# Optimization experiments

Hardware: AMD Instinct MI355X
Metric: run time of the kernel (lower is better)

Reference implementation:

```python
import jax, jax.numpy as jnp
import numpy as np

N_CODES = 8192
CODE_DIM = 256
COMMITMENT_COST = 0.25
DECAY = 0.99
EPS = 1e-05


def setup_inputs() -> dict:
    key = jax.random.key(0)
    k1, k2 = jax.random.split(key)
    z = jax.random.normal(k1, (8, 4096, CODE_DIM), dtype=jnp.float32)
    bound = 1.0 / N_CODES
    codebook_weight = jax.random.uniform(k2, (N_CODES, CODE_DIM), dtype=jnp.float32,
                                         minval=-bound, maxval=bound)
    ema_count = jnp.zeros((N_CODES,), dtype=jnp.float32)
    ema_weight = codebook_weight  # initialized as a clone of the codebook
    return {"z": z, "codebook_weight": codebook_weight,
            "ema_count": ema_count, "ema_weight": ema_weight}


def reference(z, codebook_weight, ema_count, ema_weight):
    B, L, D = z.shape
    flat_z = z.reshape(-1, D)                      # (N, D)
    # squared-distance matrix: ||z||^2 - 2 z.C^T + ||C||^2  -> (N, n_codes)
    dists = (jnp.sum(flat_z * flat_z, axis=1, keepdims=True)
             - 2.0 * flat_z @ codebook_weight.T
             + jnp.sum(codebook_weight * codebook_weight, axis=1)[None, :])
    indices = jnp.argmin(dists, axis=-1)           # (N,)
    z_q_flat = codebook_weight[indices]            # (N, D) gather

    # --- EMA codebook update (training-mode, no-grad branch) ---
    fz = jax.lax.stop_gradient(flat_z)
    count = jax.ops.segment_sum(jnp.ones_like(indices, dtype=jnp.float32),
                                indices, num_segments=N_CODES)          # one_hot.sum(0)
    new_ema_count = DECAY * ema_count + (1.0 - DECAY) * count
    weight_sum = jax.ops.segment_sum(fz, indices, num_segments=N_CODES)  # one_hot.T @ flat_z
    new_ema_weight = DECAY * ema_weight + (1.0 - DECAY) * weight_sum
    n = jnp.sum(new_ema_count)
    count_stable = (new_ema_count + EPS) / (n + N_CODES * EPS) * n
    new_codebook = new_ema_weight / count_stable[:, None]

    # --- losses + straight-through ---
    commitment_loss = jnp.mean((flat_z - jax.lax.stop_gradient(z_q_flat)) ** 2)
    vq_loss = COMMITMENT_COST * commitment_loss
    z_q_flat = flat_z + jax.lax.stop_gradient(z_q_flat - flat_z)
    z_q = z_q_flat.reshape(B, L, D)
    indices = indices.reshape(B, L)
    return (z_q, indices, vq_loss, new_codebook, new_ema_count, new_ema_weight)
```

## Files before the change

kernel.cpp:

```cpp
#include <hip/hip_runtime.h>
#include <stdint.h>

#define NROWS   32768
#define NCODES  8192
#define DIM     256
#define NSPLIT  8
#define CPS     1024
#define MAXFIX  24576
#define MAXPAIRS 262144
#define MAXRESC (MAXFIX * NSPLIT)

typedef __attribute__((ext_vector_type(8))) _Float16 f16x8;
typedef __attribute__((ext_vector_type(4))) float f32x4;

__device__ __forceinline__ f16x8 cvt8h(const float* __restrict__ p) {
    float4 a = *(const float4*)p;
    float4 b = *(const float4*)(p + 4);
    f16x8 H;
    H[0] = (_Float16)a.x; H[1] = (_Float16)a.y;
    H[2] = (_Float16)a.z; H[3] = (_Float16)a.w;
    H[4] = (_Float16)b.x; H[5] = (_Float16)b.y;
    H[6] = (_Float16)b.z; H[7] = (_Float16)b.w;
    return H;
}

__global__ __launch_bounds__(256) void k_prep(const float* __restrict__ cb,
                                              const float* __restrict__ z,
                                              unsigned short* __restrict__ bh,
                                              unsigned* __restrict__ cmax2,
                                              float* __restrict__ sum1) {
    __shared__ float zz[32 * 257];
    const int t = threadIdx.x;
    if (blockIdx.x < 1024) {
        int i = blockIdx.x * 256 + t;
        const float* p = cb + (size_t)i * 8;
        float4 a = *(const float4*)p;
        float4 b = *(const float4*)(p + 4);
        f16x8 H;
        H[0] = (_Float16)(a.x * 8192.0f); H[1] = (_Float16)(a.y * 8192.0f);
        H[2] = (_Float16)(a.z * 8192.0f); H[3] = (_Float16)(a.w * 8192.0f);
        H[4] = (_Float16)(b.x * 8192.0f); H[5] = (_Float16)(b.y * 8192.0f);
        H[6] = (_Float16)(b.z * 8192.0f); H[7] = (_Float16)(b.w * 8192.0f);
        int j = (i & ~31) | ((i & 31) ^ ((i >> 5) & 7));
        *(f16x8*)(bh + (size_t)j * 8) = H;
        float ss = a.x*a.x + a.y*a.y + a.z*a.z + a.w*a.w
                 + b.x*b.x + b.y*b.y + b.z*b.z + b.w*b.w;
        #pragma unroll
        for (int off = 1; off < 32; off <<= 1) ss += __shfl_xor(ss, off);
        if ((t & 31) == 0) atomicMax(cmax2, __float_as_uint(ss));
        return;
    }
    const int bid = blockIdx.x - 1024;
    const size_t base = (size_t)bid * 32 * 256;
    #pragma unroll
    for (int k = 0; k < 8; ++k) {
        int f4 = t + k * 256;
        float4 v = *(const float4*)(z + base + (size_t)f4 * 4);
        int row = f4 >> 6, col = (f4 & 63) * 4;
        float* d = &zz[row * 257 + col];
        d[0] = v.x * v.x; d[1] = v.y * v.y; d[2] = v.z * v.z; d[3] = v.w * v.w;
    }
    __syncthreads();
    if (t < 32) {
        const float* x = &zz[t * 257];
        float tot = 0.0f;
        #pragma unroll
        for (int h = 0; h < 2; ++h) {
            float r0 = x[0], r1 = x[1], r2 = x[2], r3 = x[3];
            float r4 = x[4], r5 = x[5], r6 = x[6], r7 = x[7];
            for (int i = 8; i < 128; i += 8) {
                r0 += x[i + 0]; r1 += x[i + 1]; r2 += x[i + 2]; r3 += x[i + 3];
                r4 += x[i + 4]; r5 += x[i + 5]; r6 += x[i + 6]; r7 += x[i + 7];
            }
            float bsum = ((r0 + r1) + (r2 + r3)) + ((r4 + r5) + (r6 + r7));
            tot = (h == 0) ? bsum : (tot + bsum);
            x += 128;
        }
        sum1[bid * 32 + t] = tot;
    }
}

__device__ __forceinline__ void stage_h(const unsigned short* __restrict__ gh,
                                        int cbase, int w, int lane,
                                        unsigned short* B) {
    const unsigned short* sh = gh + (size_t)cbase * 256;
    #pragma unroll
    for (int k = 0; k < 4; ++k) {
        const int ub = k * 256 + w * 64;
        __builtin_amdgcn_global_load_lds(
            (const __attribute__((address_space(1))) void*)(sh + (size_t)(ub + lane) * 8),
            (__attribute__((address_space(3))) void*)(B + (size_t)ub * 8), 16, 0, 0);
    }
}

__global__ __launch_bounds__(256, 2) void k_dist(
    const float* __restrict__ z,
    const unsigned short* __restrict__ bh,
    float* __restrict__ pm1, float* __restrict__ pm2, float* __restrict__ pm3)
{
    __shared__ __align__(16) unsigned short Bs[2][32][256];

    const int bid   = blockIdx.x;
    const int split = bid & (NSPLIT - 1);
    const int rt    = bid >> 3;
    const int rowbase = rt * 256;
    const int cbase0  = split * CPS;

    const int t    = threadIdx.x;
    const int w    = t >> 6;
    const int lane = t & 63;
    const int quad = lane >> 4;
    const int l15  = lane & 15;

    stage_h(bh, cbase0, w, lane, &Bs[0][0][0]);

    f16x8 Af[4][8];
    const int rbase = rowbase + w * 64;
    #pragma unroll
    for (int mt = 0; mt < 4; ++mt) {
        const float* zp = z + (size_t)(rbase + mt*16 + l15) * DIM + quad * 8;
        #pragma unroll
        for (int ks = 0; ks < 8; ++ks)
            Af[mt][ks] = cvt8h(zp + ks * 32);
    }

    int offB[2][8];
    #pragma unroll
    for (int nt = 0; nt < 2; ++nt) {
        const int cc = nt * 16 + l15;
        const int cx = cc & 7;
        #pragma unroll
        for (int ks = 0; ks < 8; ++ks)
            offB[nt][ks] = cc * 512 + (((quad + 4 * ks) ^ cx) * 16);
    }
    const unsigned idx0 = 8191u - (unsigned)(cbase0 + l15);

    float m1[16], m2[16], m3[16];
    #pragma unroll
    for (int s = 0; s < 16; ++s) { m1[s] = -3.4e38f; m2[s] = -3.4e38f; m3[s] = -3.4e38f; }

    __syncthreads();

#define KD_ROUND(RND, BCUR, BNXT)                                               \
    {                                                                           \
        if ((RND) + 1 < CPS / 32)                                               \
            stage_h(bh, cbase0 + ((RND) + 1) * 32, w, lane, (BNXT));            \
        const char* baseB = (const char*)(BCUR);                                \
        _Pragma("unroll")                                                       \
        for (int nt = 0; nt < 2; ++nt) {                                        \
            f32x4 a0 = {0,0,0,0}, a1 = {0,0,0,0}, a2 = {0,0,0,0}, a3 = {0,0,0,0};\
            _Pragma("unroll")                                                   \
            for (int ks = 0; ks < 8; ++ks) {                                    \
                f16x8 Bk = *(const f16x8*)(baseB + offB[nt][ks]);               \
                a0 = __builtin_amdgcn_mfma_f32_16x16x32_f16(Af[0][ks], Bk, a0, 0, 0, 0); \
                a1 = __builtin_amdgcn_mfma_f32_16x16x32_f16(Af[1][ks], Bk, a1, 0, 0, 0); \
                a2 = __builtin_amdgcn_mfma_f32_16x16x32_f16(Af[2][ks], Bk, a2, 0, 0, 0); \
                a3 = __builtin_amdgcn_mfma_f32_16x16x32_f16(Af[3][ks], Bk, a3, 0, 0, 0); \
            }                                                                   \
            const unsigned ibnt = idx0 - (unsigned)((RND) * 32 + nt * 16);      \
            _Pragma("unroll")                                                   \
            for (int mt = 0; mt < 4; ++mt) {                                    \
                _Pragma("unroll")                                               \
                for (int r = 0; r < 4; ++r) {                                   \
                    float dot = mt == 0 ? a0[r] : mt == 1 ? a1[r] : mt == 2 ? a2[r] : a3[r]; \
                    unsigned kb = (__float_as_uint(dot) & 0xFFFFE000u) | ibnt;  \
                    float kf = __uint_as_float(kb);                             \
                    int s = mt * 4 + r;                                         \
                    m3[s] = __builtin_amdgcn_fmed3f(m2[s], m3[s], kf);          \
                    m2[s] = __builtin_amdgcn_fmed3f(m1[s], m2[s], kf);          \
                    m1[s] = fmaxf(m1[s], kf);                                   \
                }                                                               \
            }                                                                   \
        }                                                                       \
        __syncthreads();                                                        \
    }

    for (int r2 = 0; r2 < CPS / 64; ++r2) {
        KD_ROUND(2 * r2,     &Bs[0][0][0], &Bs[1][0][0]);
        KD_ROUND(2 * r2 + 1, &Bs[1][0][0], &Bs[0][0][0]);
    }
#undef KD_ROUND

    #pragma unroll
    for (int off = 1; off < 16; off <<= 1) {
        #pragma unroll
        for (int s = 0; s < 16; ++s) {
            float o1 = __shfl_xor(m1[s], off);
            float o2 = __shfl_xor(m2[s], off);
            float o3 = __shfl_xor(m3[s], off);
            m3[s] = __builtin_amdgcn_fmed3f(m2[s], m3[s], o1);
            m2[s] = __builtin_amdgcn_fmed3f(m1[s], m2[s], o1);
            m1[s] = fmaxf(m1[s], o1);
            m3[s] = __builtin_amdgcn_fmed3f(m2[s], m3[s], o2);
            m2[s] = __builtin_amdgcn_fmed3f(m1[s], m2[s], o2);
            m1[s] = fmaxf(m1[s], o2);
            m3[s] = __builtin_amdgcn_fmed3f(m2[s], m3[s], o3);
            m2[s] = __builtin_amdgcn_fmed3f(m1[s], m2[s], o3);
            m1[s] = fmaxf(m1[s], o3);
        }
    }
    if (l15 == 0) {
        #pragma unroll
        for (int s = 0; s < 16; ++s) {
            int mt = s >> 2, r = s & 3;
            int row = rbase + mt * 16 + quad * 4 + r;
            pm1[row * NSPLIT + split] = m1[s];
            pm2[row * NSPLIT + split] = m2[s];
            pm3[row * NSPLIT + split] = m3[s];
        }
    }
}

__global__ void k_combine(const float* __restrict__ pm1, const float* __restrict__ pm2,
                          const float* __restrict__ pm3, const float* __restrict__ sum1,
                          const unsigned* __restrict__ cmax2,
                          int* __restrict__ idx_i, float* __restrict__ out_idx,
                          int* __restrict__ flagc, int* __restrict__ fixl,
                          float* __restrict__ fixthr, int* __restrict__ npairs,
                          int2* __restrict__ pairs, int* __restrict__ nresc,
                          int2* __restrict__ resc, int* __restrict__ count)
{
    int r = blockIdx.x * 256 + threadIdx.x;
    float a[8], b[8], c[8];
    #pragma unroll
    for (int s = 0; s < NSPLIT; ++s) {
        a[s] = pm1[r * NSPLIT + s];
        b[s] = pm2[r * NSPLIT + s];
        c[s] = pm3[r * NSPLIT + s];
    }
    float M1 = -3.4e38f, M2 = -3.4e38f;
    #pragma unroll
    for (int s = 0; s < NSPLIT; ++s) {
        M2 = fmaxf(fmaxf(M2, b[s]), fminf(M1, a[s]));
        M1 = fmaxf(M1, a[s]);
    }
    int I1 = (int)(8191u - (__float_as_uint(M1) & 8191u));
    idx_i[r] = I1;
    out_idx[r] = (float)I1;
    float cn = sqrtf(__uint_as_float(*cmax2)) * 8192.0f;
    float ds = 9.80e-4f * sqrtf(sum1[r]) * cn + 3e-3f;
    float t1 = sum1[r] - M1 * 0x1p-12f;
    unsigned eb = (__float_as_uint(t1 + 0.05f) >> 23) & 0xFFu;
    float q = __uint_as_float((eb - 23u) << 23);
    bool fixed = false;
    if (M1 - M2 <= (q + 2e-6f) * 8192.0f + 2.0f * ds + 0.0655f) {
        int p = atomicAdd(flagc, 1);
        if (p < MAXFIX) {
            fixed = true;
            fixl[p] = r;
            float thr = M1 - ((1.25f * q + 4e-6f) * 8192.0f + 2.2f * ds + 0.16f);
            fixthr[p] = thr;
            #pragma unroll
            for (int s = 0; s < NSPLIT; ++s) {
                if (a[s] >= thr) {
                    int pp = atomicAdd(npairs, 1);
                    if (pp < MAXPAIRS)
                        pairs[pp] = make_int2(p, (int)(8191u - (__float_as_uint(a[s]) & 8191u)));
                }
                if (b[s] >= thr) {
                    int pp = atomicAdd(npairs, 1);
                    if (pp < MAXPAIRS)
                        pairs[pp] = make_int2(p, (int)(8191u - (__float_as_uint(b[s]) & 8191u)));
                }
                if (c[s] >= thr) {
                    int pp = atomicAdd(npairs, 1);
                    if (pp < MAXPAIRS)
                        pairs[pp] = make_int2(p, (int)(8191u - (__float_as_uint(c[s]) & 8191u)));
                    int q2 = atomicAdd(nresc, 1);
                    if (q2 < MAXRESC) resc[q2] = make_int2(p, s);
                }
            }
        }
    }
    if (!fixed) atomicAdd(&count[I1], 1);
}

__global__ __launch_bounds__(256) void k_resc(
    const float* __restrict__ z, const float* __restrict__ cb,
    const int* __restrict__ nresc_p, const int2* __restrict__ resc,
    const int* __restrict__ fixl, const float* __restrict__ fixthr,
    int* __restrict__ npairs, int2* __restrict__ pairs)
{
    int nr = *nresc_p; if (nr > MAXRESC) nr = MAXRESC;
    const int w = threadIdx.x >> 6, lane = threadIdx.x & 63;
    for (int it = blockIdx.x; it < nr; it += gridDim.x) {
        const int slot = resc[it].x, split = resc[it].y;
        const int row = fixl[slot];
        const float thr = fixthr[slot];
        float4 zv = *(const float4*)(z + (size_t)row * DIM + lane * 4);
        const int cbase = split * CPS + w * 256;
        for (int cc = 0; cc < 256; cc += 4) {
            const float* cp = cb + (size_t)(cbase + cc) * DIM + lane * 4;
            float4 c0 = *(const float4*)(cp);
            float4 c1 = *(const float4*)(cp + DIM);
            float4 c2 = *(const float4*)(cp + 2 * DIM);
            float4 c3 = *(const float4*)(cp + 3 * DIM);
            float d0 = zv.x*c0.x + zv.y*c0.y + zv.z*c0.z + zv.w*c0.w;
            float d1 = zv.x*c1.x + zv.y*c1.y + zv.z*c1.z + zv.w*c1.w;
            float d2 = zv.x*c2.x + zv.y*c2.y + zv.z*c2.z + zv.w*c2.w;
            float d3 = zv.x*c3.x + zv.y*c3.y + zv.z*c3.z + zv.w*c3.w;
            #pragma unroll
            for (int off = 1; off < 64; off <<= 1) {
                d0 += __shfl_xor(d0, off);
                d1 += __shfl_xor(d1, off);
                d2 += __shfl_xor(d2, off);
                d3 += __shfl_xor(d3, off);
            }
            if (lane == 0) {
                if (d0 * 8192.0f >= thr) {
                    int pp = atomicAdd(npairs, 1);
                    if (pp < MAXPAIRS) pairs[pp] = make_int2(slot, cbase + cc);
                }
                if (d1 * 8192.0f >= thr) {
                    int pp = atomicAdd(npairs, 1);
                    if (pp < MAXPAIRS) pairs[pp] = make_int2(slot, cbase + cc + 1);
                }
                if (d2 * 8192.0f >= thr) {
                    int pp = atomicAdd(npairs, 1);
                    if (pp < MAXPAIRS) pairs[pp] = make_int2(slot, cbase + cc + 2);
                }
                if (d3 * 8192.0f >= thr) {
                    int pp = atomicAdd(npairs, 1);
                    if (pp < MAXPAIRS) pairs[pp] = make_int2(slot, cbase + cc + 3);
                }
            }
        }
    }
}

__global__ __launch_bounds__(256) void k_exact(
    const float* __restrict__ z, const float* __restrict__ cb,
    const float* __restrict__ sum1, const int* __restrict__ npairs_p,
    const int2* __restrict__ pairs, const int* __restrict__ fixl,
    unsigned long long* __restrict__ slotkey)
{
    int np = *npairs_p; if (np > MAXPAIRS) np = MAXPAIRS;
    const int lane = threadIdx.x & 63;
    const int wid = blockIdx.x * 4 + (threadIdx.x >> 6);
    for (int p = wid; p < np; p += gridDim.x * 4) {
        const int slot = pairs[p].x, code = pairs[p].y;
        const int row = fixl[slot];
        float4 a = *(const float4*)(z  + (size_t)row  * DIM + lane * 4);
        float4 c = *(const float4*)(cb + (size_t)code * DIM + lane * 4);
        double d = (double)a.x * (double)c.x + (double)a.y * (double)c.y
                 + (double)a.z * (double)c.z + (double)a.w * (double)c.w;
        #pragma unroll
        for (int off = 1; off < 64; off <<= 1) d += __shfl_xor(d, off);
        if (lane == 0) {
            float v = sum1[row] - 2.0f * (float)d;
            unsigned long long key =
                ((unsigned long long)__float_as_uint(v) << 32) | (unsigned)code;
            atomicMin(&slotkey[slot], key);
        }
    }
}

__global__ void k_fin(const int* __restrict__ flagc, const int* __restrict__ fixl,
                      const unsigned long long* __restrict__ slotkey,
                      int* __restrict__ idx_i, float* __restrict__ out_idx,
                      int* __restrict__ count)
{
    int nf = *flagc; if (nf > MAXFIX) nf = MAXFIX;
    int slot = blockIdx.x * 256 + threadIdx.x;
    if (slot >= nf) return;
    int r = fixl[slot];
    unsigned long long key = slotkey[slot];
    int idx;
    if (key != ~0ull) {
        idx = (int)(key & 0xFFFFFFFFull) & (NCODES - 1);
        idx_i[r] = idx;
        out_idx[r] = (float)idx;
    } else {
        idx = idx_i[r] & (NCODES - 1);
    }
    atomicAdd(&count[idx], 1);
}

__global__ __launch_bounds__(256) void k_prefix(const int* __restrict__ count,
                                                const float* __restrict__ in_ec,
                                                int* __restrict__ binstart,
                                                int* __restrict__ bincur,
                                                float* __restrict__ necs,
                                                float* __restrict__ out_nec,
                                                float* __restrict__ n_cell)
{
    __shared__ int ts[257];
    __shared__ float red[256];
    const int t = threadIdx.x;
    int local[32];
    int s = 0;
    float ecs = 0.0f;
    #pragma unroll
    for (int k = 0; k < 32; ++k) {
        int i = t * 32 + k;
        local[k] = count[i];
        s += local[k];
        float e = in_ec[i];
        ecs += e;
        float nec = fmaf(0.99f, e, 0.01f * (float)local[k]);
        necs[i] = nec;
        out_nec[i] = nec;
    }
    ts[t + 1] = s;
    if (t == 0) ts[0] = 0;
    red[t] = ecs;
    __syncthreads();
    for (int off = 1; off < 256; off <<= 1) {
        int v = (t >= off) ? ts[t + 1 - off] : 0;
        __syncthreads();
        ts[t + 1] += v;
        __syncthreads();
    }
    int base = ts[t];
    #pragma unroll
    for (int k = 0; k < 32; ++k) {
        int i = t * 32 + k;
        binstart[i] = base;
        bincur[i]   = base;
        base += local[k];
    }
    for (int off = 128; off > 0; off >>= 1) {
        __syncthreads();
        if (t < off) red[t] += red[t + off];
    }
    __syncthreads();
    if (t == 0) *n_cell = fmaf(0.99f, red[0], 0.01f * 32768.0f);
}

__global__ void k_place(const int* __restrict__ idx_i, int* __restrict__ bincur,
                        int* __restrict__ sorted)
{
    int row = blockIdx.x * 256 + threadIdx.x;
    int idx = idx_i[row] & (NCODES - 1);
    int pos = atomicAdd(&bincur[idx], 1);
    sorted[pos] = row;
}

__global__ __launch_bounds__(256) void k_wg(
    const float* __restrict__ z, const float* __restrict__ cb,
    const int* __restrict__ binstart, const int* __restrict__ count,
    const int* __restrict__ sorted, const float* __restrict__ in_ew,
    const float* __restrict__ necs, const float* __restrict__ n_cell,
    float* __restrict__ lossp, int* __restrict__ done,
    float* __restrict__ out_zq, float* __restrict__ out_ncb,
    float* __restrict__ out_new, float* __restrict__ out_loss)
{
    __shared__ int islast;
    __shared__ float lred[128];
    const int w = threadIdx.x >> 6, lane = threadIdx.x & 63;
    const int code = blockIdx.x * 4 + w;
    const int s0 = binstart[code], cnt = count[code];
    const int d0 = lane * 4;
    float4 cv = *(const float4*)(cb + (size_t)code * DIM + d0);
    float4 ws = {0.f, 0.f, 0.f, 0.f};
    float ls = 0.0f;
    int k = 0;
    for (; k + 2 <= cnt; k += 2) {
        int ra = sorted[s0 + k], rb = sorted[s0 + k + 1];
        float4 va = *(const float4*)(z + (size_t)ra * DIM + d0);
        float4 vb = *(const float4*)(z + (size_t)rb * DIM + d0);
        *(float4*)(out_zq + (size_t)ra * DIM + d0) = cv;
        *(float4*)(out_zq + (size_t)rb * DIM + d0) = cv;
        ws.x += va.x + vb.x; ws.y += va.y + vb.y;
        ws.z += va.z + vb.z; ws.w += va.w + vb.w;
        float ax = va.x - cv.x, ay = va.y - cv.y, az = va.z - cv.z, aw = va.w - cv.w;
        float bx = vb.x - cv.x, by = vb.y - cv.y, bz = vb.z - cv.z, bw = vb.w - cv.w;
        ls += ax*ax + ay*ay + az*az + aw*aw + bx*bx + by*by + bz*bz + bw*bw;
    }
    if (k < cnt) {
        int ra = sorted[s0 + k];
        float4 va = *(const float4*)(z + (size_t)ra * DIM + d0);
        *(float4*)(out_zq + (size_t)ra * DIM + d0) = cv;
        ws.x += va.x; ws.y += va.y; ws.z += va.z; ws.w += va.w;
        float ax = va.x - cv.x, ay = va.y - cv.y, az = va.z - cv.z, aw = va.w - cv.w;
        ls += ax*ax + ay*ay + az*az + aw*aw;
    }
    #pragma unroll
    for (int off = 1; off < 64; off <<= 1) ls += __shfl_xor(ls, off);
    if (lane == 0) atomicAdd(&lossp[code & 127], ls);

    size_t o = (size_t)code * DIM + d0;
    float4 ew4 = *(const float4*)(in_ew + o);
    float n = *n_cell;
    float nec = necs[code];
    float cs = (nec + 1e-5f) / (n + (float)NCODES * 1e-5f) * n;
    float4 nw, nc;
    nw.x = fmaf(0.99f, ew4.x, 0.01f * ws.x); nc.x = nw.x / cs;
    nw.y = fmaf(0.99f, ew4.y, 0.01f * ws.y); nc.y = nw.y / cs;
    nw.z = fmaf(0.99f, ew4.z, 0.01f * ws.z); nc.z = nw.z / cs;
    nw.w = fmaf(0.99f, ew4.w, 0.01f * ws.w); nc.w = nw.w / cs;
    *(float4*)(out_new + o) = nw;
    *(float4*)(out_ncb + o) = nc;

    __syncthreads();
    if (threadIdx.x == 0) {
        __threadfence();
        islast = (atomicAdd(done, 1) == (int)gridDim.x - 1) ? 1 : 0;
    }
    __syncthreads();
    if (islast) {
        if (threadIdx.x < 128) lred[threadIdx.x] = atomicAdd(&lossp[threadIdx.x], 0.0f);
        __syncthreads();
        if (threadIdx.x == 0) {
            float s = 0.f;
            for (int i = 0; i < 128; ++i) s += lred[i];
            out_loss[0] = 0.25f * s / 8388608.0f;
        }
    }
}

extern "C" void kernel_launch(void* const* d_in, const int* in_sizes, int n_in,
                              void* d_out, int out_size, void* d_ws, size_t ws_size,
                              hipStream_t stream)
{
    const float* z  = nullptr;
    const float* cb = nullptr;
    const float* ec = nullptr;
    const float* ew = nullptr;
    for (int i = 0; i < n_in; ++i) {
        if (in_sizes[i] == NROWS * DIM)       z  = (const float*)d_in[i];
        else if (in_sizes[i] == NCODES)       ec = (const float*)d_in[i];
        else if (in_sizes[i] == NCODES * DIM) { if (!cb) cb = (const float*)d_in[i]; else ew = (const float*)d_in[i]; }
    }
    if (!z)  z  = (const float*)d_in[0];
    if (!cb) cb = (const float*)d_in[1];
    if (!ec) ec = (const float*)d_in[2];
    if (!ew) ew = cb;
    float* out = (float*)d_out;

    char* ws = (char*)d_ws;
    int*    count   = (int*)   (ws + 0);
    float*  lossp   = (float*) (ws + 32768);
    float*  n_cell  = (float*) (ws + 33280);
    int*    flagc   = (int*)   (ws + 33284);
    int*    npairs  = (int*)   (ws + 33288);
    unsigned* cmax2 = (unsigned*)(ws + 33292);
    int*    nresc   = (int*)   (ws + 33296);
    int*    done    = (int*)   (ws + 33300);
    float*  sum1    = (float*) (ws + 33312);
    float*  pm1     = (float*) (ws + 164384);
    float*  pm2     = (float*) (ws + 1212960);
    float*  pm3     = (float*) (ws + 2261536);
    int*    fixl    = (int*)   (ws + 3310112);
    float*  fixthr  = (float*) (ws + 3408416);
    unsigned long long* slotkey = (unsigned long long*)(ws + 3506720);
    int2*   pairs   = (int2*)  (ws + 3703328);
    int2*   resc    = (int2*)  (ws + 5800480);
    int*    idx_i   = (int*)   (ws + 7373344);
    float*  necs    = (float*) (ws + 7504416);
    int*    binstart= (int*)   (ws + 7537184);
    int*    bincur  = (int*)   (ws + 7569952);
    int*    sorted  = (int*)   (ws + 7602720);
    unsigned short* bh_g = (unsigned short*)(ws + 7733792);

    float* out_zq   = out;
    float* out_idx  = out + 8388608;
    float* out_loss = out + 8421376;
    float* out_ncb  = out + 8421377;
    float* out_nec  = out + 10518529;
    float* out_new  = out + 10526721;

    hipMemsetAsync(d_ws, 0, 33312, stream);
    hipMemsetAsync(slotkey, 0xFF, (size_t)MAXFIX * 8, stream);
    k_prep   <<<2048,  256, 0, stream>>>(cb, z, bh_g, cmax2, sum1);
    k_dist   <<<1024,  256, 0, stream>>>(z, bh_g, pm1, pm2, pm3);
    k_combine<<<128,   256, 0, stream>>>(pm1, pm2, pm3, sum1, cmax2, idx_i, out_idx,
                                         flagc, fixl, fixthr, npairs, pairs, nresc, resc,
                                         count);
    k_resc   <<<512,   256, 0, stream>>>(z, cb, nresc, resc, fixl, fixthr, npairs, pairs);
    k_exact  <<<4096,  256, 0, stream>>>(z, cb, sum1, npairs, pairs, fixl, slotkey);
    k_fin    <<<96,    256, 0, stream>>>(flagc, fixl, slotkey, idx_i, out_idx, count);
    k_prefix <<<1,     256, 0, stream>>>(count, ec, binstart, bincur, necs, out_nec, n_cell);
    k_place  <<<128,   256, 0, stream>>>(idx_i, bincur, sorted);
    k_wg     <<<NCODES/4, 256, 0, stream>>>(z, cb, binstart, count, sorted, ew, necs,
                                            n_cell, lossp, done, out_zq, out_ncb,
                                            out_new, out_loss);
}
```

Baseline: 550.4 us.

## Triple-buffer codebook staging in distance kernel with explicit vmcnt waits

Moves the LDS staging of codebook tiles in the distance kernel from double to triple buffering, prefetching two tiles ahead. Each round waits with an explicit s_waitcnt vmcnt and a single barrier instead of a barrier after compute. The per-nt offset array is collapsed into one array plus a constant offset to save registers. The third buffer raises LDS use per block, which may affect occupancy, and the hand-written vmcnt counts must match the number of outstanding loads.

Measured after the change: 552.1 us. About the same (+0.3%).

```diff
diff --git a/kernel.cpp b/kernel.cpp
--- a/kernel.cpp
+++ b/kernel.cpp
@@ -98,7 +98,7 @@
     const unsigned short* __restrict__ bh,
     float* __restrict__ pm1, float* __restrict__ pm2, float* __restrict__ pm3)
 {
-    __shared__ __align__(16) unsigned short Bs[2][32][256];
+    __shared__ __align__(16) unsigned short Bs[3][32][256];
 
     const int bid   = blockIdx.x;
     const int split = bid & (NSPLIT - 1);
@@ -112,7 +112,8 @@
     const int quad = lane >> 4;
     const int l15  = lane & 15;
 
-    stage_h(bh, cbase0, w, lane, &Bs[0][0][0]);
+    stage_h(bh, cbase0 + 0 * 32, w, lane, &Bs[0][0][0]);
+    stage_h(bh, cbase0 + 1 * 32, w, lane, &Bs[1][0][0]);
 
     f16x8 Af[4][8];
     const int rbase = rowbase + w * 64;
@@ -124,34 +125,25 @@
             Af[mt][ks] = cvt8h(zp + ks * 32);
     }
 
-    int offB[2][8];
-    #pragma unroll
-    for (int nt = 0; nt < 2; ++nt) {
-        const int cc = nt * 16 + l15;
-        const int cx = cc & 7;
-        #pragma unroll
-        for (int ks = 0; ks < 8; ++ks)
-            offB[nt][ks] = cc * 512 + (((quad + 4 * ks) ^ cx) * 16);
-    }
+    int offB[8];
+    const int cx = l15 & 7;
+    #pragma unroll
+    for (int ks = 0; ks < 8; ++ks)
+        offB[ks] = l15 * 512 + (((quad + 4 * ks) ^ cx) * 16);
     const unsigned idx0 = 8191u - (unsigned)(cbase0 + l15);
 
     float m1[16], m2[16], m3[16];
     #pragma unroll
     for (int s = 0; s < 16; ++s) { m1[s] = -3.4e38f; m2[s] = -3.4e38f; m3[s] = -3.4e38f; }
 
-    __syncthreads();
-
-#define KD_ROUND(RND, BCUR, BNXT)                                               \
-    {                                                                           \
-        if ((RND) + 1 < CPS / 32)                                               \
-            stage_h(bh, cbase0 + ((RND) + 1) * 32, w, lane, (BNXT));            \
-        const char* baseB = (const char*)(BCUR);                                \
+#define KD_BODY(RND, BREAD)                                                     \
+        const char* baseB = (const char*)(BREAD);                               \
         _Pragma("unroll")                                                       \
         for (int nt = 0; nt < 2; ++nt) {                                        \
             f32x4 a0 = {0,0,0,0}, a1 = {0,0,0,0}, a2 = {0,0,0,0}, a3 = {0,0,0,0};\
             _Pragma("unroll")                                                   \
             for (int ks = 0; ks < 8; ++ks) {                                    \
-                f16x8 Bk = *(const f16x8*)(baseB + offB[nt][ks]);               \
+                f16x8 Bk = *(const f16x8*)(baseB + offB[ks] + nt * 8192);       \
                 a0 = __builtin_amdgcn_mfma_f32_16x16x32_f16(Af[0][ks], Bk, a0, 0, 0, 0); \
                 a1 = __builtin_amdgcn_mfma_f32_16x16x32_f16(Af[1][ks], Bk, a1, 0, 0, 0); \
                 a2 = __builtin_amdgcn_mfma_f32_16x16x32_f16(Af[2][ks], Bk, a2, 0, 0, 0); \
@@ -171,15 +163,40 @@
                     m1[s] = fmaxf(m1[s], kf);                                   \
                 }                                                               \
             }                                                                   \
-        }                                                                       \
-        __syncthreads();                                                        \
-    }
-
-    for (int r2 = 0; r2 < CPS / 64; ++r2) {
-        KD_ROUND(2 * r2,     &Bs[0][0][0], &Bs[1][0][0]);
-        KD_ROUND(2 * r2 + 1, &Bs[1][0][0], &Bs[0][0][0]);
-    }
+        }
+
+#define KD_ROUND(RND, BREAD, BISSUE)                                            \
+    {                                                                           \
+        __builtin_amdgcn_sched_barrier(0);                                      \
+        asm volatile("s_waitcnt vmcnt(4)" ::: "memory");                        \
+        __builtin_amdgcn_s_barrier();                                           \
+        __builtin_amdgcn_sched_barrier(0);                                      \
+        stage_h(bh, cbase0 + ((RND) + 2) * 32, w, lane, (BISSUE));              \
+        KD_BODY(RND, BREAD)                                                     \
+    }
+
+#define KD_TAIL(RND, BREAD, VMC)                                                \
+    {                                                                           \
+        __builtin_amdgcn_sched_barrier(0);                                      \
+        asm volatile("s_waitcnt vmcnt(" VMC ")" ::: "memory");                  \
+        __builtin_amdgcn_s_barrier();                                           \
+        __builtin_amdgcn_sched_barrier(0);                                      \
+        KD_BODY(RND, BREAD)                                                     \
+    }
+
+    #pragma unroll 1
+    for (int r3 = 0; r3 < 10; ++r3) {
+        const int r = r3 * 3;
+        KD_ROUND(r,     &Bs[0][0][0], &Bs[2][0][0]);
+        KD_ROUND(r + 1, &Bs[1][0][0], &Bs[0][0][0]);
+        KD_ROUND(r + 2, &Bs[2][0][0], &Bs[1][0][0]);
+    }
+    KD_TAIL(30, &Bs[0][0][0], "4");
+    KD_TAIL(31, &Bs[1][0][0], "0");
+
 #undef KD_ROUND
+#undef KD_TAIL
+#undef KD_BODY
 
     #pragma unroll
     for (int off = 1; off < 16; off <<= 1) {
```

## Aggregate combine-kernel atomics per wavefront and fold slotkey init into combine

Applied to the files above, without the earlier changes.

Replaces the per-thread atomicAdd on the fix counter and the pair counter with wavefront-level ballot/popcount and prefix-scan reservations, so each wave issues one atomic per counter. The slotkey reset memset is dropped and each fixed slot is initialised inside the combine kernel instead. The exact-distance kernel grid is also halved. This lowers atomic contention and removes one memset launch, but the pair ordering changes and the halved grid may reduce parallelism in k_exact.

Result: faster. 483.3 us (-12.2%).

```diff
diff --git a/kernel.cpp b/kernel.cpp
--- a/kernel.cpp
+++ b/kernel.cpp
@@ -218,9 +218,11 @@
                           int* __restrict__ flagc, int* __restrict__ fixl,
                           float* __restrict__ fixthr, int* __restrict__ npairs,
                           int2* __restrict__ pairs, int* __restrict__ nresc,
-                          int2* __restrict__ resc, int* __restrict__ count)
+                          int2* __restrict__ resc, int* __restrict__ count,
+                          unsigned long long* __restrict__ slotkey)
 {
     int r = blockIdx.x * 256 + threadIdx.x;
+    const int lane = threadIdx.x & 63;
     float a[8], b[8], c[8];
     #pragma unroll
     for (int s = 0; s < NSPLIT; ++s) {
@@ -242,33 +244,67 @@
     float t1 = sum1[r] - M1 * 0x1p-12f;
     unsigned eb = (__float_as_uint(t1 + 0.05f) >> 23) & 0xFFu;
     float q = __uint_as_float((eb - 23u) << 23);
-    bool fixed = false;
-    if (M1 - M2 <= (q + 2e-6f) * 8192.0f + 2.0f * ds + 0.0655f) {
-        int p = atomicAdd(flagc, 1);
-        if (p < MAXFIX) {
-            fixed = true;
-            fixl[p] = r;
-            float thr = M1 - ((1.25f * q + 4e-6f) * 8192.0f + 2.2f * ds + 0.16f);
-            fixthr[p] = thr;
-            #pragma unroll
-            for (int s = 0; s < NSPLIT; ++s) {
-                if (a[s] >= thr) {
-                    int pp = atomicAdd(npairs, 1);
-                    if (pp < MAXPAIRS)
-                        pairs[pp] = make_int2(p, (int)(8191u - (__float_as_uint(a[s]) & 8191u)));
-                }
-                if (b[s] >= thr) {
-                    int pp = atomicAdd(npairs, 1);
-                    if (pp < MAXPAIRS)
-                        pairs[pp] = make_int2(p, (int)(8191u - (__float_as_uint(b[s]) & 8191u)));
-                }
-                if (c[s] >= thr) {
-                    int pp = atomicAdd(npairs, 1);
-                    if (pp < MAXPAIRS)
-                        pairs[pp] = make_int2(p, (int)(8191u - (__float_as_uint(c[s]) & 8191u)));
-                    int q2 = atomicAdd(nresc, 1);
-                    if (q2 < MAXRESC) resc[q2] = make_int2(p, s);
-                }
+    bool want = (M1 - M2 <= (q + 2e-6f) * 8192.0f + 2.0f * ds + 0.0655f);
+
+    unsigned long long wm = __ballot(want);
+    int base = 0;
+    if (wm != 0ull) {
+        if (lane == 0) base = atomicAdd(flagc, (int)__popcll(wm));
+        base = __shfl(base, 0);
+    }
+    int p = base + (int)__popcll(wm & ((1ull << lane) - 1ull));
+    bool fixed = want && (p < MAXFIX);
+
+    float thr = 0.0f;
+    int ecnt = 0;
+    bool ea[8], ebb[8], ecc[8];
+    #pragma unroll
+    for (int s = 0; s < NSPLIT; ++s) { ea[s] = false; ebb[s] = false; ecc[s] = false; }
+    if (fixed) {
+        fixl[p] = r;
+        thr = M1 - ((1.25f * q + 4e-6f) * 8192.0f + 2.2f * ds + 0.16f);
+        fixthr[p] = thr;
+        slotkey[p] = ~0ull;
+        #pragma unroll
+        for (int s = 0; s < NSPLIT; ++s) {
+            ea[s]  = (a[s] >= thr);
+            ebb[s] = (b[s] >= thr);
+            ecc[s] = (c[s] >= thr);
+            ecnt += (int)ea[s] + (int)ebb[s] + (int)ecc[s];
+        }
+    }
+    int off = ecnt;
+    #pragma unroll
+    for (int d = 1; d < 64; d <<= 1) {
+        int o = __shfl_up(off, d);
+        if (lane >= d) off += o;
+    }
+    int tot = __shfl(off, 63);
+    int pb = 0;
+    if (tot > 0) {
+        if (lane == 63) pb = atomicAdd(npairs, tot);
+        pb = __shfl(pb, 63);
+    }
+    int wpos = pb + off - ecnt;
+    if (fixed) {
+        #pragma unroll
+        for (int s = 0; s < NSPLIT; ++s) {
+            if (ea[s]) {
+                if (wpos < MAXPAIRS)
+                    pairs[wpos] = make_int2(p, (int)(8191u - (__float_as_uint(a[s]) & 8191u)));
+                ++wpos;
+            }
+            if (ebb[s]) {
+                if (wpos < MAXPAIRS)
+                    pairs[wpos] = make_int2(p, (int)(8191u - (__float_as_uint(b[s]) & 8191u)));
+                ++wpos;
+            }
+            if (ecc[s]) {
+                if (wpos < MAXPAIRS)
+                    pairs[wpos] = make_int2(p, (int)(8191u - (__float_as_uint(c[s]) & 8191u)));
+                ++wpos;
+                int q2 = atomicAdd(nresc, 1);
+                if (q2 < MAXRESC) resc[q2] = make_int2(p, s);
             }
         }
     }
@@ -561,14 +597,13 @@
     float* out_new  = out + 10526721;
 
     hipMemsetAsync(d_ws, 0, 33312, stream);
-    hipMemsetAsync(slotkey, 0xFF, (size_t)MAXFIX * 8, stream);
     k_prep   <<<2048,  256, 0, stream>>>(cb, z, bh_g, cmax2, sum1);
     k_dist   <<<1024,  256, 0, stream>>>(z, bh_g, pm1, pm2, pm3);
     k_combine<<<128,   256, 0, stream>>>(pm1, pm2, pm3, sum1, cmax2, idx_i, out_idx,
                                          flagc, fixl, fixthr, npairs, pairs, nresc, resc,
-                                         count);
+                                         count, slotkey);
     k_resc   <<<512,   256, 0, stream>>>(z, cb, nresc, resc, fixl, fixthr, npairs, pairs);
-    k_exact  <<<4096,  256, 0, stream>>>(z, cb, sum1, npairs, pairs, fixl, slotkey);
+    k_exact  <<<2048,  256, 0, stream>>>(z, cb, sum1, npairs, pairs, fixl, slotkey);
     k_fin    <<<96,    256, 0, stream>>>(flagc, fixl, slotkey, idx_i, out_idx, count);
     k_prefix <<<1,     256, 0, stream>>>(count, ec, binstart, bincur, necs, out_nec, n_cell);
     k_place  <<<128,   256, 0, stream>>>(idx_i, bincur, sorted);
```
